# Optimization experiments

Hardware: AMD Instinct MI355X
Metric: run time of the kernel (lower is better)

Reference implementation:

```python
import jax, jax.numpy as jnp
import numpy as np

EPS = 1e-5

def _ln(x, g, b):
    mu = jnp.mean(x, axis=-1, keepdims=True)
    var = jnp.var(x, axis=-1, keepdims=True)
    return (x - mu) * jax.lax.rsqrt(var + EPS) * g + b

def setup_inputs() -> dict:
    key = jax.random.key(0)
    ks = jax.random.split(key, 12)
    T, B, D, H = 64, 2048, 512, 512
    seq = jax.random.normal(ks[0], (T, B, D), dtype=jnp.float32)
    ts = jnp.sort(jax.random.uniform(ks[1], (B, T), dtype=jnp.float32) * 10.0, axis=1)
    def xavier(k, shape):
        fan_in, fan_out = shape[1], shape[0]
        lim = float(np.sqrt(6.0 / (fan_in + fan_out)))
        return jax.random.uniform(k, shape, jnp.float32, -lim, lim)
    Wr = xavier(ks[2], (H, D + H)); br = jnp.ones((H,), jnp.float32)   # reset bias init 1.0
    Wz = xavier(ks[3], (H, D + H)); bz = jnp.ones((H,), jnp.float32)   # update bias init 1.0
    Wc = xavier(ks[4], (H, D + H)); bc = jnp.zeros((H,), jnp.float32)
    Wo = xavier(ks[5], (H, H));     bo = jnp.zeros((H,), jnp.float32)  # output projection
    gx = jnp.ones((D,), jnp.float32); bx = jnp.zeros((D,), jnp.float32)  # layer_norm_x
    gh = jnp.ones((H,), jnp.float32); bh = jnp.zeros((H,), jnp.float32)  # layer_norm_h
    gc = jnp.ones((H,), jnp.float32); bcell = jnp.zeros((H,), jnp.float32)  # layer_norm_out (cell)
    gf = jnp.ones((H,), jnp.float32); bf = jnp.zeros((H,), jnp.float32)  # final layer_norm
    return {"seq": seq, "time_stamps": ts,
            "Wr": Wr, "br": br, "Wz": Wz, "bz": bz, "Wc": Wc, "bc": bc,
            "Wo": Wo, "bo": bo, "gx": gx, "bx": bx, "gh": gh, "bh": bh,
            "gc": gc, "bcell": bcell, "gf": gf, "bf": bf}

def _cell(xn, hn, Wr, br, Wz, bz, Wc, bc, gc, bcell):
    # xn: normalized input [B,D]; hn: (normalized, time-scaled) hidden [B,H]
    xh = jnp.concatenate([xn, hn], axis=-1)
    r = jax.nn.sigmoid(xh @ Wr.T + br)
    z = jax.nn.sigmoid(xh @ Wz.T + bz)
    xrh = jnp.concatenate([xn, r * hn], axis=-1)
    h_tilde = jnp.tanh(xrh @ Wc.T + bc)
    h_new = (1.0 - z) * hn + z * h_tilde
    return _ln(h_new, gc, bcell)  # cell output layer norm (dropout is identity in eval)

def reference(seq, time_stamps, Wr, br, Wz, bz, Wc, bc, Wo, bo, gx, bx, gh, bh, gc, bcell, gf, bf):
    T, B, D = seq.shape
    # first step: h is None -> zeros, no LN on h, no time-decay
    x0 = _ln(seq[0], gx, bx)
    h0 = _cell(x0, jnp.zeros((B, Wr.shape[0]), seq.dtype), Wr, br, Wz, bz, Wc, bc, gc, bcell)
    # remaining steps under scan with LN(h) and exp(-dt) decay
    dts = (time_stamps[:, 1:] - time_stamps[:, :-1]).T  # [T-1, B]
    def step(h, inp):
        x_t, dt = inp
        xn = _ln(x_t, gx, bx)
        hn = _ln(h, gh, bh) * jnp.exp(-jnp.clip(dt, 0.0, 10.0))[:, None]
        h_new = _cell(xn, hn, Wr, br, Wz, bz, Wc, bc, gc, bcell)
        return h_new, h_new
    _, rest = jax.lax.scan(step, h0, (seq[1:], dts))
    states = jnp.concatenate([h0[None], rest], axis=0)  # [T,B,H]
    out = jnp.einsum('tbh,oh->tbo', states, Wo) + bo
    out = out + seq  # residual (input_dim == hidden_dim); dropout identity in eval
    return _ln(out, gf, bf)
```

## Files before the change

### kernel.cpp

```cpp
#include <hip/hip_runtime.h>
#include <math.h>

#define TT 64
#define BB 2048

using f32x4   = __attribute__((ext_vector_type(4))) float;
using short8  = __attribute__((ext_vector_type(8))) short;
using short4v = __attribute__((ext_vector_type(4))) short;

__device__ __forceinline__ unsigned short f2bf(float f) {
    unsigned u = __float_as_uint(f);
    u += 0x7FFF + ((u >> 16) & 1);
    return (unsigned short)(u >> 16);
}
__device__ __forceinline__ float bf2f(unsigned short h) {
    return __uint_as_float(((unsigned)h) << 16);
}
__device__ __forceinline__ float sigmoidf_(float v) { return 1.0f / (1.0f + expf(-v)); }
__device__ __forceinline__ float tanhf_(float v)    { return 1.0f - 2.0f / (expf(2.0f * v) + 1.0f); }

__global__ __launch_bounds__(256)
void cvt_kernel(const float* __restrict__ src, unsigned short* __restrict__ dst, int n) {
    int i = blockIdx.x * 256 + threadIdx.x;
    if (i < n) dst[i] = f2bf(src[i]);
}

__global__ __launch_bounds__(256)
void pack_w2(const float* __restrict__ src, unsigned short* __restrict__ dst,
             int N, int Ksrc, int kbeg, int Kpk) {
    int i = blockIdx.x * 256 + threadIdx.x;
    if (i >= N * Kpk) return;
    int n = i / Kpk, k = i - n * Kpk;
    int dstIdx = ((n >> 4) * (Kpk >> 5) + (k >> 5)) * 512 + (((k >> 3) & 3) * 16 + (n & 15)) * 8 + (k & 7);
    dst[dstIdx] = f2bf(src[(size_t)n * Ksrc + kbeg + k]);
}

__device__ __forceinline__ int pk_idx(int row, int col) {
    int ks = col >> 5, khi = (col >> 3) & 3, j = col & 7;
    return ((ks * 64) + khi * 16 + row) * 8 + j;
}

__device__ __forceinline__ void ln_row_pk(const float* __restrict__ xr,
                                          const float* __restrict__ g,
                                          const float* __restrict__ b,
                                          unsigned short* __restrict__ tile,
                                          int row, int lane) {
    const int c0 = lane * 8;
    float4 v0 = *(const float4*)(xr + c0);
    float4 v1 = *(const float4*)(xr + c0 + 4);
    float s  = v0.x + v0.y + v0.z + v0.w + v1.x + v1.y + v1.z + v1.w;
    float ss = v0.x*v0.x + v0.y*v0.y + v0.z*v0.z + v0.w*v0.w
             + v1.x*v1.x + v1.y*v1.y + v1.z*v1.z + v1.w*v1.w;
#pragma unroll
    for (int m = 32; m > 0; m >>= 1) { s += __shfl_xor(s, m); ss += __shfl_xor(ss, m); }
    const float mean = s * (1.0f / 512.0f);
    const float var  = ss * (1.0f / 512.0f) - mean * mean;
    const float rs   = rsqrtf(var + 1e-5f);
    float4 g0 = *(const float4*)(g + c0);
    float4 g1 = *(const float4*)(g + c0 + 4);
    float4 b0 = *(const float4*)(b + c0);
    float4 b1 = *(const float4*)(b + c0 + 4);
    short8 o;
    o[0] = (short)f2bf((v0.x - mean) * rs * g0.x + b0.x);
    o[1] = (short)f2bf((v0.y - mean) * rs * g0.y + b0.y);
    o[2] = (short)f2bf((v0.z - mean) * rs * g0.z + b0.z);
    o[3] = (short)f2bf((v0.w - mean) * rs * g0.w + b0.w);
    o[4] = (short)f2bf((v1.x - mean) * rs * g1.x + b1.x);
    o[5] = (short)f2bf((v1.y - mean) * rs * g1.y + b1.y);
    o[6] = (short)f2bf((v1.z - mean) * rs * g1.z + b1.z);
    o[7] = (short)f2bf((v1.w - mean) * rs * g1.w + b1.w);
    *(short8*)&tile[(((lane >> 2) * 64) + (lane & 3) * 16 + row) * 8] = o;
}

__global__ __launch_bounds__(512)
void gx_kernel(const float* __restrict__ seq, const float* __restrict__ gxw,
               const float* __restrict__ bxw, const unsigned short* __restrict__ Wx3,
               unsigned short* __restrict__ gx)
{
    __shared__ unsigned short xt[4 * 8192];
    const int tid  = threadIdx.x;
    const int w    = tid >> 6;
    const int lane = tid & 63;
    const size_t m0 = (size_t)blockIdx.x * 64;
    const int t    = (int)(m0 >> 11);
    const int bloc = (int)((m0 & 2047) >> 4);

#pragma unroll
    for (int rr = 0; rr < 8; ++rr) {
        const int r = w * 8 + rr;
        ln_row_pk(seq + (m0 + r) * 512, gxw, bxw, xt + (r >> 4) * 8192, r & 15, lane);
    }
    __syncthreads();

    for (int nt = 0; nt < 3; ++nt) {
        f32x4 acc[4][4] = {};
#pragma unroll 4
        for (int ks = 0; ks < 16; ++ks) {
            short8 a[4], b[4];
#pragma unroll
            for (int mf = 0; mf < 4; ++mf)
                a[mf] = *(const short8*)&xt[mf * 8192 + (ks * 64 + lane) * 8];
#pragma unroll
            for (int nf = 0; nf < 4; ++nf)
                b[nf] = *(const short8*)(Wx3 + (size_t)(nt * 32 + w * 4 + nf) * 8192 + ks * 512 + lane * 8);
#pragma unroll
            for (int mf = 0; mf < 4; ++mf)
#pragma unroll
                for (int nf = 0; nf < 4; ++nf)
                    acc[mf][nf] = __builtin_amdgcn_mfma_f32_16x16x32_bf16(a[mf], b[nf], acc[mf][nf], 0, 0, 0);
        }
#pragma unroll
        for (int mf = 0; mf < 4; ++mf)
#pragma unroll
            for (int nf = 0; nf < 4; ++nf) {
                const size_t base = (((size_t)t * 128 + bloc + mf) * 96 + nt * 32 + w * 4 + nf) * 256 + lane * 4;
                short4v o;
                o[0] = (short)f2bf(acc[mf][nf][0]);
                o[1] = (short)f2bf(acc[mf][nf][1]);
                o[2] = (short)f2bf(acc[mf][nf][2]);
                o[3] = (short)f2bf(acc[mf][nf][3]);
                *(short4v*)&gx[base] = o;
            }
    }
}

template<int SBF, int HOIST>
__global__ __launch_bounds__(512)
void recurrent_kernel(const float* __restrict__ seq, const float* __restrict__ ts,
                      const unsigned short* __restrict__ Wrz, const unsigned short* __restrict__ Wc,
                      const float* __restrict__ br, const float* __restrict__ bz,
                      const float* __restrict__ bc,
                      const float* __restrict__ gxw, const float* __restrict__ bxw,
                      const float* __restrict__ gh, const float* __restrict__ bh,
                      const float* __restrict__ gc, const float* __restrict__ bcl,
                      const unsigned short* __restrict__ gx,
                      float* __restrict__ states_f32, unsigned short* __restrict__ states_bf)
{
    __shared__ unsigned short hn_s[16 * 512];
    __shared__ unsigned short rh_s[16 * 512];
    __shared__ unsigned short xn_s[HOIST ? 64 : 16 * 512];
    __shared__ float red_s[16][8];
    __shared__ float red_q[16][8];

    const int tid  = threadIdx.x;
    const int w    = tid >> 6;
    const int lane = tid & 63;
    const int lhi  = lane >> 4;
    const int llo  = lane & 15;
    const int m0   = blockIdx.x * 16;

    for (int i = tid; i < 1024; i += 512) *(short8*)&hn_s[i * 8] = short8{};
    if (!HOIST) {
#pragma unroll
        for (int rr = 0; rr < 2; ++rr) {
            const int r = w * 2 + rr;
            ln_row_pk(seq + (size_t)(m0 + r) * 512, gxw, bxw, xn_s, r, lane);
        }
    }
    __syncthreads();

    float zreg[4][4];

    for (int t = 0; t < TT; ++t) {
        const unsigned short* gxt = HOIST ? gx + (((size_t)t * 128 + blockIdx.x) * 96) * 256 + lane * 4 : nullptr;

        {
            f32x4 aR[4] = {}, aZ[4] = {};
            if (HOIST) {
#pragma unroll
                for (int f = 0; f < 4; ++f) {
                    short4v g1 = *(const short4v*)(gxt + (size_t)(w * 4 + f) * 256);
                    short4v g2 = *(const short4v*)(gxt + (size_t)(32 + w * 4 + f) * 256);
#pragma unroll
                    for (int i = 0; i < 4; ++i) {
                        aR[f][i] = bf2f((unsigned short)g1[i]);
                        aZ[f][i] = bf2f((unsigned short)g2[i]);
                    }
                }
#pragma unroll 4
                for (int ks = 0; ks < 16; ++ks) {
                    short8 a = *(const short8*)&hn_s[(ks * 64 + lane) * 8];
                    const int off = ks * 512 + lane * 8;
#pragma unroll
                    for (int f = 0; f < 4; ++f) {
                        short8 b1 = *(const short8*)(Wrz + (size_t)(w * 4 + f) * 8192 + off);
                        aR[f] = __builtin_amdgcn_mfma_f32_16x16x32_bf16(a, b1, aR[f], 0, 0, 0);
                        short8 b2 = *(const short8*)(Wrz + (size_t)(32 + w * 4 + f) * 8192 + off);
                        aZ[f] = __builtin_amdgcn_mfma_f32_16x16x32_bf16(a, b2, aZ[f], 0, 0, 0);
                    }
                }
            } else {
                const unsigned short* wrb = Wrz + (size_t)(w * 4) * 16384;
                const unsigned short* wzb = Wrz + (size_t)(32 + w * 4) * 16384;
#pragma unroll 4
                for (int ks = 0; ks < 16; ++ks) {
                    short8 a = *(const short8*)&xn_s[(ks * 64 + lane) * 8];
                    const int off = ks * 512 + lane * 8;
#pragma unroll
                    for (int f = 0; f < 4; ++f) {
                        short8 b1 = *(const short8*)(wrb + (size_t)f * 16384 + off);
                        aR[f] = __builtin_amdgcn_mfma_f32_16x16x32_bf16(a, b1, aR[f], 0, 0, 0);
                        short8 b2 = *(const short8*)(wzb + (size_t)f * 16384 + off);
                        aZ[f] = __builtin_amdgcn_mfma_f32_16x16x32_bf16(a, b2, aZ[f], 0, 0, 0);
                    }
                }
#pragma unroll 4
                for (int ks = 16; ks < 32; ++ks) {
                    short8 a = *(const short8*)&hn_s[((ks - 16) * 64 + lane) * 8];
                    const int off = ks * 512 + lane * 8;
#pragma unroll
                    for (int f = 0; f < 4; ++f) {
                        short8 b1 = *(const short8*)(wrb + (size_t)f * 16384 + off);
                        aR[f] = __builtin_amdgcn_mfma_f32_16x16x32_bf16(a, b1, aR[f], 0, 0, 0);
                        short8 b2 = *(const short8*)(wzb + (size_t)f * 16384 + off);
                        aZ[f] = __builtin_amdgcn_mfma_f32_16x16x32_bf16(a, b2, aZ[f], 0, 0, 0);
                    }
                }
            }
#pragma unroll
            for (int f = 0; f < 4; ++f)
#pragma unroll
                for (int i = 0; i < 4; ++i) {
                    const int row = lhi * 4 + i;
                    const int col = w * 64 + f * 16 + llo;
                    const float rr = sigmoidf_(aR[f][i] + br[col]);
                    const float hv = bf2f(hn_s[pk_idx(row, col)]);
                    rh_s[pk_idx(row, col)] = f2bf(rr * hv);
                    zreg[f][i] = sigmoidf_(aZ[f][i] + bz[col]);
                }
        }
        __syncthreads();

        f32x4 aC[4] = {};
        {
            if (HOIST) {
#pragma unroll
                for (int f = 0; f < 4; ++f) {
                    short4v g3 = *(const short4v*)(gxt + (size_t)(64 + w * 4 + f) * 256);
#pragma unroll
                    for (int i = 0; i < 4; ++i) aC[f][i] = bf2f((unsigned short)g3[i]);
                }
#pragma unroll 4
                for (int ks = 0; ks < 16; ++ks) {
                    short8 a = *(const short8*)&rh_s[(ks * 64 + lane) * 8];
                    const int off = ks * 512 + lane * 8;
#pragma unroll
                    for (int f = 0; f < 4; ++f) {
                        short8 b1 = *(const short8*)(Wc + (size_t)(w * 4 + f) * 8192 + off);
                        aC[f] = __builtin_amdgcn_mfma_f32_16x16x32_bf16(a, b1, aC[f], 0, 0, 0);
                    }
                }
            } else {
                const unsigned short* wcb = Wc + (size_t)(w * 4) * 16384;
#pragma unroll 4
                for (int ks = 0; ks < 16; ++ks) {
                    short8 a = *(const short8*)&xn_s[(ks * 64 + lane) * 8];
                    const int off = ks * 512 + lane * 8;
#pragma unroll
                    for (int f = 0; f < 4; ++f) {
                        short8 b1 = *(const short8*)(wcb + (size_t)f * 16384 + off);
                        aC[f] = __builtin_amdgcn_mfma_f32_16x16x32_bf16(a, b1, aC[f], 0, 0, 0);
                    }
                }
#pragma unroll 4
                for (int ks = 16; ks < 32; ++ks) {
                    short8 a = *(const short8*)&rh_s[((ks - 16) * 64 + lane) * 8];
                    const int off = ks * 512 + lane * 8;
#pragma unroll
                    for (int f = 0; f < 4; ++f) {
                        short8 b1 = *(const short8*)(wcb + (size_t)f * 16384 + off);
                        aC[f] = __builtin_amdgcn_mfma_f32_16x16x32_bf16(a, b1, aC[f], 0, 0, 0);
                    }
                }
            }
        }
        __syncthreads();

        {
            float hnew[4][4];
#pragma unroll
            for (int f = 0; f < 4; ++f)
#pragma unroll
                for (int i = 0; i < 4; ++i) {
                    const int row = lhi * 4 + i;
                    const int col = w * 64 + f * 16 + llo;
                    const float htil = tanhf_(aC[f][i] + bc[col]);
                    const float hv = bf2f(hn_s[pk_idx(row, col)]);
                    const float z = zreg[f][i];
                    hnew[f][i] = (1.0f - z) * hv + z * htil;
                }
#pragma unroll
            for (int i = 0; i < 4; ++i) {
                float s = hnew[0][i] + hnew[1][i] + hnew[2][i] + hnew[3][i];
                float q = hnew[0][i]*hnew[0][i] + hnew[1][i]*hnew[1][i]
                        + hnew[2][i]*hnew[2][i] + hnew[3][i]*hnew[3][i];
#pragma unroll
                for (int m = 8; m >= 1; m >>= 1) { s += __shfl_xor(s, m); q += __shfl_xor(q, m); }
                if (llo == 0) { red_s[lhi * 4 + i][w] = s; red_q[lhi * 4 + i][w] = q; }
            }
            __syncthreads();
            float mu[4], rsd[4];
#pragma unroll
            for (int i = 0; i < 4; ++i) {
                float s = 0.f, q = 0.f;
#pragma unroll
                for (int w2 = 0; w2 < 8; ++w2) { s += red_s[lhi * 4 + i][w2]; q += red_q[lhi * 4 + i][w2]; }
                const float m_ = s * (1.0f / 512.0f);
                mu[i]  = m_;
                rsd[i] = rsqrtf(q * (1.0f / 512.0f) - m_ * m_ + 1e-5f);
            }
#pragma unroll
            for (int f = 0; f < 4; ++f)
#pragma unroll
                for (int i = 0; i < 4; ++i) {
                    const int row = lhi * 4 + i;
                    const int col = w * 64 + f * 16 + llo;
                    const float h = (hnew[f][i] - mu[i]) * rsd[i] * gc[col] + bcl[col];
                    const size_t off = (size_t)t * BB * 512 + (size_t)(m0 + row) * 512 + col;
                    if (SBF) states_bf[off] = f2bf(h);
                    else     states_f32[off] = h;
                    hnew[f][i] = h;
                }
            if (t + 1 < TT) {
                __syncthreads();
#pragma unroll
                for (int i = 0; i < 4; ++i) {
                    float s = hnew[0][i] + hnew[1][i] + hnew[2][i] + hnew[3][i];
                    float q = hnew[0][i]*hnew[0][i] + hnew[1][i]*hnew[1][i]
                            + hnew[2][i]*hnew[2][i] + hnew[3][i]*hnew[3][i];
#pragma unroll
                    for (int m = 8; m >= 1; m >>= 1) { s += __shfl_xor(s, m); q += __shfl_xor(q, m); }
                    if (llo == 0) { red_s[lhi * 4 + i][w] = s; red_q[lhi * 4 + i][w] = q; }
                }
                __syncthreads();
                float dec_[4];
#pragma unroll
                for (int i = 0; i < 4; ++i) {
                    float s = 0.f, q = 0.f;
#pragma unroll
                    for (int w2 = 0; w2 < 8; ++w2) { s += red_s[lhi * 4 + i][w2]; q += red_q[lhi * 4 + i][w2]; }
                    const float m_ = s * (1.0f / 512.0f);
                    mu[i]  = m_;
                    rsd[i] = rsqrtf(q * (1.0f / 512.0f) - m_ * m_ + 1e-5f);
                    const int row = m0 + lhi * 4 + i;
                    float dtv = ts[(size_t)row * TT + t + 1] - ts[(size_t)row * TT + t];
                    dtv = fminf(fmaxf(dtv, 0.0f), 10.0f);
                    dec_[i] = expf(-dtv);
                }
#pragma unroll
                for (int f = 0; f < 4; ++f)
#pragma unroll
                    for (int i = 0; i < 4; ++i) {
                        const int row = lhi * 4 + i;
                        const int col = w * 64 + f * 16 + llo;
                        const float hv = ((hnew[f][i] - mu[i]) * rsd[i] * gh[col] + bh[col]) * dec_[i];
                        hn_s[pk_idx(row, col)] = f2bf(hv);
                    }
                if (!HOIST) {
#pragma unroll
                    for (int rr = 0; rr < 2; ++rr) {
                        const int r = w * 2 + rr;
                        ln_row_pk(seq + ((size_t)(t + 1) * BB + m0 + r) * 512, gxw, bxw, xn_s, r, lane);
                    }
                }
            }
        }
        __syncthreads();
    }
}

template<int BF>
__global__ __launch_bounds__(512)
void proj_kernel(const float* __restrict__ S, const unsigned short* __restrict__ Sb,
                 const unsigned short* __restrict__ Wo, const float* __restrict__ bo,
                 const float* __restrict__ seq, const float* __restrict__ gf,
                 const float* __restrict__ bff, float* __restrict__ out)
{
    const int tid  = threadIdx.x;
    const int wave = tid >> 6;
    const int lane = tid & 63;
    const int lhi  = lane >> 4;
    const int llo  = lane & 15;
    const long m0  = (long)blockIdx.x * 64;

    f32x4 acc[4][4] = {};
    for (int k0 = 0; k0 < 512; k0 += 32) {
        const int kk = k0 + lhi * 8;
        short8 a[4], b[4];
#pragma unroll
        for (int mf = 0; mf < 4; ++mf) {
            if (BF) {
                a[mf] = *(const short8*)(Sb + (size_t)(m0 + mf * 16 + llo) * 512 + kk);
            } else {
                const float* ap = S + (size_t)(m0 + mf * 16 + llo) * 512 + kk;
                float4 f0 = *(const float4*)ap;
                float4 f1 = *(const float4*)(ap + 4);
                short8 av;
                av[0] = (short)f2bf(f0.x); av[1] = (short)f2bf(f0.y);
                av[2] = (short)f2bf(f0.z); av[3] = (short)f2bf(f0.w);
                av[4] = (short)f2bf(f1.x); av[5] = (short)f2bf(f1.y);
                av[6] = (short)f2bf(f1.z); av[7] = (short)f2bf(f1.w);
                a[mf] = av;
            }
        }
#pragma unroll
        for (int nf = 0; nf < 4; ++nf)
            b[nf] = *(const short8*)(Wo + (size_t)(wave * 64 + nf * 16 + llo) * 512 + kk);
#pragma unroll
        for (int mf = 0; mf < 4; ++mf)
#pragma unroll
            for (int nf = 0; nf < 4; ++nf)
                acc[mf][nf] = __builtin_amdgcn_mfma_f32_16x16x32_bf16(a[mf], b[nf], acc[mf][nf], 0, 0, 0);
    }

    __shared__ float red_s[64][8];
    __shared__ float red_q[64][8];

#pragma unroll
    for (int mf = 0; mf < 4; ++mf)
#pragma unroll
        for (int i = 0; i < 4; ++i) {
            const long row = m0 + mf * 16 + lhi * 4 + i;
#pragma unroll
            for (int nf = 0; nf < 4; ++nf) {
                const int col = wave * 64 + nf * 16 + llo;
                acc[mf][nf][i] += bo[col] + seq[(size_t)row * 512 + col];
            }
        }
    float mu[4][4], rstd[4][4];
#pragma unroll
    for (int mf = 0; mf < 4; ++mf)
#pragma unroll
        for (int i = 0; i < 4; ++i) {
            float s = 0.f, q = 0.f;
#pragma unroll
            for (int nf = 0; nf < 4; ++nf) { const float v = acc[mf][nf][i]; s += v; q += v * v; }
#pragma unroll
            for (int m = 8; m >= 1; m >>= 1) { s += __shfl_xor(s, m); q += __shfl_xor(q, m); }
            if (llo == 0) { red_s[mf * 16 + lhi * 4 + i][wave] = s; red_q[mf * 16 + lhi * 4 + i][wave] = q; }
        }
    __syncthreads();
#pragma unroll
    for (int mf = 0; mf < 4; ++mf)
#pragma unroll
        for (int i = 0; i < 4; ++i) {
            const int rl = mf * 16 + lhi * 4 + i;
            float s = 0.f, q = 0.f;
#pragma unroll
            for (int w2 = 0; w2 < 8; ++w2) { s += red_s[rl][w2]; q += red_q[rl][w2]; }
            const float m_ = s * (1.0f / 512.0f);
            const float var = q * (1.0f / 512.0f) - m_ * m_;
            mu[mf][i] = m_;
            rstd[mf][i] = rsqrtf(var + 1e-5f);
        }
#pragma unroll
    for (int mf = 0; mf < 4; ++mf)
#pragma unroll
        for (int i = 0; i < 4; ++i) {
            const long row = m0 + mf * 16 + lhi * 4 + i;
#pragma unroll
            for (int nf = 0; nf < 4; ++nf) {
                const int col = wave * 64 + nf * 16 + llo;
                out[(size_t)row * 512 + col] = (acc[mf][nf][i] - mu[mf][i]) * rstd[mf][i] * gf[col] + bff[col];
            }
        }
}

extern "C" void kernel_launch(void* const* d_in, const int* in_sizes, int n_in,
                              void* d_out, int out_size, void* d_ws, size_t ws_size,
                              hipStream_t stream) {
    const float* seq = (const float*)d_in[0];
    const float* ts  = (const float*)d_in[1];
    const float* Wr  = (const float*)d_in[2];
    const float* br  = (const float*)d_in[3];
    const float* Wz  = (const float*)d_in[4];
    const float* bz  = (const float*)d_in[5];
    const float* Wc  = (const float*)d_in[6];
    const float* bc  = (const float*)d_in[7];
    const float* Wo  = (const float*)d_in[8];
    const float* bo  = (const float*)d_in[9];
    const float* gx  = (const float*)d_in[10];
    const float* bx  = (const float*)d_in[11];
    const float* gh  = (const float*)d_in[12];
    const float* bh  = (const float*)d_in[13];
    const float* gc  = (const float*)d_in[14];
    const float* bcl = (const float*)d_in[15];
    const float* gf  = (const float*)d_in[16];
    const float* bf  = (const float*)d_in[17];
    float* out = (float*)d_out;

    char* w0 = (char*)d_ws;
    char* w = w0;
    unsigned short* Wrz_full = (unsigned short*)w; w += (size_t)1024 * 1024 * 2;
    unsigned short* Wc_full  = (unsigned short*)w; w += (size_t)512 * 1024 * 2;
    unsigned short* Wrz_h    = (unsigned short*)w; w += (size_t)1024 * 512 * 2;
    unsigned short* Wc_h     = (unsigned short*)w; w += (size_t)512 * 512 * 2;
    unsigned short* Wx3      = (unsigned short*)w; w += (size_t)1536 * 512 * 2;
    unsigned short* Wo_b     = (unsigned short*)w; w += (size_t)512 * 512 * 2;

    const size_t GXB = (size_t)TT * 128 * 96 * 256 * 2;
    const size_t SBB = (size_t)TT * BB * 512 * 2;

    const bool hoist = ws_size >= (size_t)(w - w0) + GXB;
    unsigned short* gxbuf = (unsigned short*)w;
    if (hoist) w += GXB;
    const bool sbf = ws_size >= (size_t)(w - w0) + SBB;
    unsigned short* states_bf = (unsigned short*)w;

    if (hoist) {
        pack_w2<<<1024, 256, 0, stream>>>(Wr, Wrz_h, 512, 1024, 512, 512);
        pack_w2<<<1024, 256, 0, stream>>>(Wz, Wrz_h + (size_t)512 * 512, 512, 1024, 512, 512);
        pack_w2<<<1024, 256, 0, stream>>>(Wc, Wc_h, 512, 1024, 512, 512);
        pack_w2<<<1024, 256, 0, stream>>>(Wr, Wx3, 512, 1024, 0, 512);
        pack_w2<<<1024, 256, 0, stream>>>(Wz, Wx3 + (size_t)512 * 512, 512, 1024, 0, 512);
        pack_w2<<<1024, 256, 0, stream>>>(Wc, Wx3 + (size_t)2 * 512 * 512, 512, 1024, 0, 512);
    } else {
        pack_w2<<<2048, 256, 0, stream>>>(Wr, Wrz_full, 512, 1024, 0, 1024);
        pack_w2<<<2048, 256, 0, stream>>>(Wz, Wrz_full + (size_t)512 * 1024, 512, 1024, 0, 1024);
        pack_w2<<<2048, 256, 0, stream>>>(Wc, Wc_full, 512, 1024, 0, 1024);
    }
    cvt_kernel<<<(512 * 512 + 255) / 256, 256, 0, stream>>>(Wo, Wo_b, 512 * 512);

    if (hoist)
        gx_kernel<<<2048, 512, 0, stream>>>(seq, gx, bx, Wx3, gxbuf);

    const unsigned short* Wa = hoist ? Wrz_h : Wrz_full;
    const unsigned short* Wb = hoist ? Wc_h  : Wc_full;
    if (hoist) {
        if (sbf) recurrent_kernel<1,1><<<128, 512, 0, stream>>>(seq, ts, Wa, Wb, br, bz, bc, gx, bx, gh, bh, gc, bcl, gxbuf, out, states_bf);
        else     recurrent_kernel<0,1><<<128, 512, 0, stream>>>(seq, ts, Wa, Wb, br, bz, bc, gx, bx, gh, bh, gc, bcl, gxbuf, out, states_bf);
    } else {
        if (sbf) recurrent_kernel<1,0><<<128, 512, 0, stream>>>(seq, ts, Wa, Wb, br, bz, bc, gx, bx, gh, bh, gc, bcl, gxbuf, out, states_bf);
        else     recurrent_kernel<0,0><<<128, 512, 0, stream>>>(seq, ts, Wa, Wb, br, bz, bc, gx, bx, gh, bh, gc, bcl, gxbuf, out, states_bf);
    }

    if (sbf)
        proj_kernel<1><<<2048, 512, 0, stream>>>(out, states_bf, Wo_b, bo, seq, gf, bf, out);
    else
        proj_kernel<0><<<2048, 512, 0, stream>>>(out, nullptr, Wo_b, bo, seq, gf, bf, out);
}
```

Baseline: 1.877 ms.

## Restructure recurrent step: overlap Z/C GEMMs, fuse dual layernorm, pack states for MFMA

The hoisted recurrent kernel now computes R first, then runs the Z and C gate GEMMs in one loop after a single barrier. It keeps hn in registers and computes both the cell layernorm and the next-step hidden layernorm from a single fused reduction, using precomputed gamma/beta moment sums, which removes a reduction round and its barriers per timestep. States are written in the MFMA-packed bf16 layout via coalesced LDS copies, and Wo is packed the same way, so the projection kernel loads contiguous fragments. The algebraic second-layernorm statistics can lose precision through catastrophic cancellation, and register pressure rises.

New measurement: 3.147 ms. +67.7%, slower.

```diff
diff --git a/kernel.cpp b/kernel.cpp
--- a/kernel.cpp
+++ b/kernel.cpp
@@ -18,12 +18,6 @@
 }
 __device__ __forceinline__ float sigmoidf_(float v) { return 1.0f / (1.0f + expf(-v)); }
 __device__ __forceinline__ float tanhf_(float v)    { return 1.0f - 2.0f / (expf(2.0f * v) + 1.0f); }
-
-__global__ __launch_bounds__(256)
-void cvt_kernel(const float* __restrict__ src, unsigned short* __restrict__ dst, int n) {
-    int i = blockIdx.x * 256 + threadIdx.x;
-    if (i < n) dst[i] = f2bf(src[i]);
-}
 
 __global__ __launch_bounds__(256)
 void pack_w2(const float* __restrict__ src, unsigned short* __restrict__ dst,
@@ -124,23 +118,20 @@
     }
 }
 
-template<int SBF, int HOIST>
+template<int SBF>
 __global__ __launch_bounds__(512)
-void recurrent_kernel(const float* __restrict__ seq, const float* __restrict__ ts,
-                      const unsigned short* __restrict__ Wrz, const unsigned short* __restrict__ Wc,
-                      const float* __restrict__ br, const float* __restrict__ bz,
-                      const float* __restrict__ bc,
-                      const float* __restrict__ gxw, const float* __restrict__ bxw,
-                      const float* __restrict__ gh, const float* __restrict__ bh,
-                      const float* __restrict__ gc, const float* __restrict__ bcl,
-                      const unsigned short* __restrict__ gx,
-                      float* __restrict__ states_f32, unsigned short* __restrict__ states_bf)
+void recurrent_h(const float* __restrict__ ts,
+                 const unsigned short* __restrict__ Wrz, const unsigned short* __restrict__ Wc,
+                 const float* __restrict__ br_, const float* __restrict__ bz_, const float* __restrict__ bc_,
+                 const float* __restrict__ gh_, const float* __restrict__ bh_,
+                 const float* __restrict__ gc_, const float* __restrict__ bcl_,
+                 const unsigned short* __restrict__ gx,
+                 float* __restrict__ states_f32, unsigned short* __restrict__ states_pk)
 {
     __shared__ unsigned short hn_s[16 * 512];
     __shared__ unsigned short rh_s[16 * 512];
-    __shared__ unsigned short xn_s[HOIST ? 64 : 16 * 512];
-    __shared__ float red_s[16][8];
-    __shared__ float red_q[16][8];
+    __shared__ float red6[6][16][9];
+    __shared__ float cpart[5][8];
 
     const int tid  = threadIdx.x;
     const int w    = tid >> 6;
@@ -148,75 +139,242 @@
     const int lhi  = lane >> 4;
     const int llo  = lane & 15;
     const int m0   = blockIdx.x * 16;
+    const int blk  = blockIdx.x;
+
+    *(short8*)&hn_s[tid * 16] = short8{};
+    *(short8*)&hn_s[tid * 16 + 8] = short8{};
+
+    {
+        float g = gc_[tid], b = bcl_[tid];
+        float p[5] = { g, b, g * g, g * b, b * b };
+#pragma unroll
+        for (int m = 32; m > 0; m >>= 1)
+#pragma unroll
+            for (int k = 0; k < 5; ++k) p[k] += __shfl_xor(p[k], m);
+        if (lane == 0)
+#pragma unroll
+            for (int k = 0; k < 5; ++k) cpart[k][w] = p[k];
+    }
+    __syncthreads();
+    float C_gc = 0.f, C_bcl = 0.f, C_g2 = 0.f, C_gb = 0.f, C_b2 = 0.f;
+#pragma unroll
+    for (int w2 = 0; w2 < 8; ++w2) {
+        C_gc += cpart[0][w2]; C_bcl += cpart[1][w2]; C_g2 += cpart[2][w2];
+        C_gb += cpart[3][w2]; C_b2 += cpart[4][w2];
+    }
+
+    float brr[4], bzr[4], bcr[4], gcr[4], bclr[4], ghr[4], bhr[4], g2r[4], gbr[4];
+#pragma unroll
+    for (int f = 0; f < 4; ++f) {
+        const int col = w * 64 + f * 16 + llo;
+        brr[f] = br_[col]; bzr[f] = bz_[col]; bcr[f] = bc_[col];
+        gcr[f] = gc_[col]; bclr[f] = bcl_[col];
+        ghr[f] = gh_[col]; bhr[f] = bh_[col];
+        g2r[f] = gcr[f] * gcr[f]; gbr[f] = gcr[f] * bclr[f];
+    }
+
+    float hnreg[4][4] = {};
+
+    for (int t = 0; t < TT; ++t) {
+        if (SBF && t > 0) {
+            unsigned short* dst = states_pk + ((size_t)(t - 1) * 128 + blk) * 8192 + (size_t)(w * 128 + lane * 2) * 8;
+            const unsigned short* srcl = &rh_s[(w * 128 + lane * 2) * 8];
+            short8 s0 = *(const short8*)srcl;
+            short8 s1 = *(const short8*)(srcl + 8);
+            *(short8*)dst = s0;
+            *(short8*)(dst + 8) = s1;
+        }
+
+        const unsigned short* gxt = gx + ((size_t)t * 128 + blk) * 96 * 256 + lane * 4;
+        short4v gR[4], gZ[4], gC[4];
+#pragma unroll
+        for (int f = 0; f < 4; ++f) {
+            gR[f] = *(const short4v*)(gxt + (size_t)(w * 4 + f) * 256);
+            gZ[f] = *(const short4v*)(gxt + (size_t)(32 + w * 4 + f) * 256);
+            gC[f] = *(const short4v*)(gxt + (size_t)(64 + w * 4 + f) * 256);
+        }
+
+        f32x4 aR[4];
+#pragma unroll
+        for (int f = 0; f < 4; ++f)
+#pragma unroll
+            for (int i = 0; i < 4; ++i) aR[f][i] = bf2f((unsigned short)gR[f][i]);
+#pragma unroll 4
+        for (int ks = 0; ks < 16; ++ks) {
+            short8 a = *(const short8*)&hn_s[(ks * 64 + lane) * 8];
+            const int off = ks * 512 + lane * 8;
+#pragma unroll
+            for (int f = 0; f < 4; ++f) {
+                short8 b1 = *(const short8*)(Wrz + (size_t)(w * 4 + f) * 8192 + off);
+                aR[f] = __builtin_amdgcn_mfma_f32_16x16x32_bf16(a, b1, aR[f], 0, 0, 0);
+            }
+        }
+#pragma unroll
+        for (int f = 0; f < 4; ++f)
+#pragma unroll
+            for (int i = 0; i < 4; ++i) {
+                const int row = lhi * 4 + i;
+                const int col = w * 64 + f * 16 + llo;
+                const float rr = sigmoidf_(aR[f][i] + brr[f]);
+                rh_s[pk_idx(row, col)] = f2bf(rr * hnreg[f][i]);
+            }
+        __syncthreads();
+
+        f32x4 aZ[4], aC[4];
+#pragma unroll
+        for (int f = 0; f < 4; ++f)
+#pragma unroll
+            for (int i = 0; i < 4; ++i) {
+                aZ[f][i] = bf2f((unsigned short)gZ[f][i]);
+                aC[f][i] = bf2f((unsigned short)gC[f][i]);
+            }
+#pragma unroll 4
+        for (int ks = 0; ks < 16; ++ks) {
+            short8 ah = *(const short8*)&hn_s[(ks * 64 + lane) * 8];
+            short8 ar = *(const short8*)&rh_s[(ks * 64 + lane) * 8];
+            const int off = ks * 512 + lane * 8;
+#pragma unroll
+            for (int f = 0; f < 4; ++f) {
+                short8 b1 = *(const short8*)(Wrz + (size_t)(32 + w * 4 + f) * 8192 + off);
+                aZ[f] = __builtin_amdgcn_mfma_f32_16x16x32_bf16(ah, b1, aZ[f], 0, 0, 0);
+                short8 b2 = *(const short8*)(Wc + (size_t)(w * 4 + f) * 8192 + off);
+                aC[f] = __builtin_amdgcn_mfma_f32_16x16x32_bf16(ar, b2, aC[f], 0, 0, 0);
+            }
+        }
+
+        float hnew[4][4];
+#pragma unroll
+        for (int f = 0; f < 4; ++f)
+#pragma unroll
+            for (int i = 0; i < 4; ++i) {
+                const float z    = sigmoidf_(aZ[f][i] + bzr[f]);
+                const float htil = tanhf_(aC[f][i] + bcr[f]);
+                hnew[f][i] = (1.0f - z) * hnreg[f][i] + z * htil;
+            }
+#pragma unroll
+        for (int i = 0; i < 4; ++i) {
+            float P[6] = {};
+#pragma unroll
+            for (int f = 0; f < 4; ++f) {
+                const float h = hnew[f][i];
+                P[0] += h;            P[1] += h * h;
+                P[2] += gcr[f] * h;   P[3] += g2r[f] * h;
+                P[4] += g2r[f] * h * h;
+                P[5] += gbr[f] * h;
+            }
+#pragma unroll
+            for (int m = 8; m >= 1; m >>= 1)
+#pragma unroll
+                for (int k = 0; k < 6; ++k) P[k] += __shfl_xor(P[k], m);
+            if (llo == 0)
+#pragma unroll
+                for (int k = 0; k < 6; ++k) red6[k][lhi * 4 + i][w] = P[k];
+        }
+        __syncthreads();
+
+        float mu1[4], rs1[4], mu2[4], rs2[4], dec_[4];
+#pragma unroll
+        for (int i = 0; i < 4; ++i) {
+            const int row = lhi * 4 + i;
+            float S[6] = {};
+#pragma unroll
+            for (int w2 = 0; w2 < 8; ++w2)
+#pragma unroll
+                for (int k = 0; k < 6; ++k) S[k] += red6[k][row][w2];
+            const float m1 = S[0] * (1.0f / 512.0f);
+            const float v1 = S[1] * (1.0f / 512.0f) - m1 * m1;
+            const float r1 = rsqrtf(v1 + 1e-5f);
+            mu1[i] = m1; rs1[i] = r1;
+            const float m2 = (r1 * (S[2] - m1 * C_gc) + C_bcl) * (1.0f / 512.0f);
+            const float eh2 = (r1 * r1 * (S[4] - 2.0f * m1 * S[3] + m1 * m1 * C_g2)
+                               + 2.0f * r1 * (S[5] - m1 * C_gb) + C_b2) * (1.0f / 512.0f);
+            mu2[i] = m2;
+            rs2[i] = rsqrtf(eh2 - m2 * m2 + 1e-5f);
+            if (t + 1 < TT) {
+                const int grow = m0 + row;
+                float dtv = ts[(size_t)grow * TT + t + 1] - ts[(size_t)grow * TT + t];
+                dtv = fminf(fmaxf(dtv, 0.0f), 10.0f);
+                dec_[i] = expf(-dtv);
+            }
+        }
+#pragma unroll
+        for (int f = 0; f < 4; ++f)
+#pragma unroll
+            for (int i = 0; i < 4; ++i) {
+                const int row = lhi * 4 + i;
+                const int col = w * 64 + f * 16 + llo;
+                const float n = (hnew[f][i] - mu1[i]) * rs1[i];
+                const float h = n * gcr[f] + bclr[f];
+                if (SBF) rh_s[pk_idx(row, col)] = f2bf(h);
+                else     states_f32[(size_t)t * BB * 512 + (size_t)(m0 + row) * 512 + col] = h;
+                if (t + 1 < TT) {
+                    const float hv = ((h - mu2[i]) * rs2[i] * ghr[f] + bhr[f]) * dec_[i];
+                    hnreg[f][i] = hv;
+                    hn_s[pk_idx(row, col)] = f2bf(hv);
+                }
+            }
+        __syncthreads();
+    }
+
+    if (SBF) {
+        unsigned short* dst = states_pk + ((size_t)(TT - 1) * 128 + blk) * 8192 + (size_t)(w * 128 + lane * 2) * 8;
+        const unsigned short* srcl = &rh_s[(w * 128 + lane * 2) * 8];
+        short8 s0 = *(const short8*)srcl;
+        short8 s1 = *(const short8*)(srcl + 8);
+        *(short8*)dst = s0;
+        *(short8*)(dst + 8) = s1;
+    }
+}
+
+template<int SBF>
+__global__ __launch_bounds__(512)
+void recurrent_fb(const float* __restrict__ seq, const float* __restrict__ ts,
+                  const unsigned short* __restrict__ Wrz, const unsigned short* __restrict__ Wc,
+                  const float* __restrict__ br, const float* __restrict__ bz,
+                  const float* __restrict__ bc,
+                  const float* __restrict__ gxw, const float* __restrict__ bxw,
+                  const float* __restrict__ gh, const float* __restrict__ bh,
+                  const float* __restrict__ gc, const float* __restrict__ bcl,
+                  float* __restrict__ states_f32, unsigned short* __restrict__ states_pk)
+{
+    __shared__ unsigned short hn_s[16 * 512];
+    __shared__ unsigned short rh_s[16 * 512];
+    __shared__ unsigned short xn_s[16 * 512];
+    __shared__ float red_s[16][9];
+    __shared__ float red_q[16][9];
+
+    const int tid  = threadIdx.x;
+    const int w    = tid >> 6;
+    const int lane = tid & 63;
+    const int lhi  = lane >> 4;
+    const int llo  = lane & 15;
+    const int m0   = blockIdx.x * 16;
 
     for (int i = tid; i < 1024; i += 512) *(short8*)&hn_s[i * 8] = short8{};
-    if (!HOIST) {
-#pragma unroll
-        for (int rr = 0; rr < 2; ++rr) {
-            const int r = w * 2 + rr;
-            ln_row_pk(seq + (size_t)(m0 + r) * 512, gxw, bxw, xn_s, r, lane);
-        }
+#pragma unroll
+    for (int rr = 0; rr < 2; ++rr) {
+        const int r = w * 2 + rr;
+        ln_row_pk(seq + (size_t)(m0 + r) * 512, gxw, bxw, xn_s, r, lane);
     }
     __syncthreads();
 
-    float zreg[4][4];
-
     for (int t = 0; t < TT; ++t) {
-        const unsigned short* gxt = HOIST ? gx + (((size_t)t * 128 + blockIdx.x) * 96) * 256 + lane * 4 : nullptr;
-
         {
             f32x4 aR[4] = {}, aZ[4] = {};
-            if (HOIST) {
+#pragma unroll 2
+            for (int ks = 0; ks < 32; ++ks) {
+                short8 a = (ks < 16) ? *(const short8*)&xn_s[(ks * 64 + lane) * 8]
+                                     : *(const short8*)&hn_s[((ks - 16) * 64 + lane) * 8];
+                const int off = ks * 512 + lane * 8;
 #pragma unroll
                 for (int f = 0; f < 4; ++f) {
-                    short4v g1 = *(const short4v*)(gxt + (size_t)(w * 4 + f) * 256);
-                    short4v g2 = *(const short4v*)(gxt + (size_t)(32 + w * 4 + f) * 256);
-#pragma unroll
-                    for (int i = 0; i < 4; ++i) {
-                        aR[f][i] = bf2f((unsigned short)g1[i]);
-                        aZ[f][i] = bf2f((unsigned short)g2[i]);
-                    }
-                }
-#pragma unroll 4
-                for (int ks = 0; ks < 16; ++ks) {
-                    short8 a = *(const short8*)&hn_s[(ks * 64 + lane) * 8];
-                    const int off = ks * 512 + lane * 8;
-#pragma unroll
-                    for (int f = 0; f < 4; ++f) {
-                        short8 b1 = *(const short8*)(Wrz + (size_t)(w * 4 + f) * 8192 + off);
-                        aR[f] = __builtin_amdgcn_mfma_f32_16x16x32_bf16(a, b1, aR[f], 0, 0, 0);
-                        short8 b2 = *(const short8*)(Wrz + (size_t)(32 + w * 4 + f) * 8192 + off);
-                        aZ[f] = __builtin_amdgcn_mfma_f32_16x16x32_bf16(a, b2, aZ[f], 0, 0, 0);
-                    }
-                }
-            } else {
-                const unsigned short* wrb = Wrz + (size_t)(w * 4) * 16384;
-                const unsigned short* wzb = Wrz + (size_t)(32 + w * 4) * 16384;
-#pragma unroll 4
-                for (int ks = 0; ks < 16; ++ks) {
-                    short8 a = *(const short8*)&xn_s[(ks * 64 + lane) * 8];
-                    const int off = ks * 512 + lane * 8;
-#pragma unroll
-                    for (int f = 0; f < 4; ++f) {
-                        short8 b1 = *(const short8*)(wrb + (size_t)f * 16384 + off);
-                        aR[f] = __builtin_amdgcn_mfma_f32_16x16x32_bf16(a, b1, aR[f], 0, 0, 0);
-                        short8 b2 = *(const short8*)(wzb + (size_t)f * 16384 + off);
-                        aZ[f] = __builtin_amdgcn_mfma_f32_16x16x32_bf16(a, b2, aZ[f], 0, 0, 0);
-                    }
-                }
-#pragma unroll 4
-                for (int ks = 16; ks < 32; ++ks) {
-                    short8 a = *(const short8*)&hn_s[((ks - 16) * 64 + lane) * 8];
-                    const int off = ks * 512 + lane * 8;
-#pragma unroll
-                    for (int f = 0; f < 4; ++f) {
-                        short8 b1 = *(const short8*)(wrb + (size_t)f * 16384 + off);
-                        aR[f] = __builtin_amdgcn_mfma_f32_16x16x32_bf16(a, b1, aR[f], 0, 0, 0);
-                        short8 b2 = *(const short8*)(wzb + (size_t)f * 16384 + off);
-                        aZ[f] = __builtin_amdgcn_mfma_f32_16x16x32_bf16(a, b2, aZ[f], 0, 0, 0);
-                    }
-                }
-            }
+                    short8 b1 = *(const short8*)(Wrz + (size_t)(w * 4 + f) * 16384 + off);
+                    aR[f] = __builtin_amdgcn_mfma_f32_16x16x32_bf16(a, b1, aR[f], 0, 0, 0);
+                    short8 b2 = *(const short8*)(Wrz + (size_t)(32 + w * 4 + f) * 16384 + off);
+                    aZ[f] = __builtin_amdgcn_mfma_f32_16x16x32_bf16(a, b2, aZ[f], 0, 0, 0);
+                }
+            }
+            float zreg[4][4];
 #pragma unroll
             for (int f = 0; f < 4; ++f)
 #pragma unroll
@@ -228,55 +386,22 @@
                     rh_s[pk_idx(row, col)] = f2bf(rr * hv);
                     zreg[f][i] = sigmoidf_(aZ[f][i] + bz[col]);
                 }
-        }
-        __syncthreads();
-
-        f32x4 aC[4] = {};
-        {
-            if (HOIST) {
+            __syncthreads();
+
+            f32x4 aC[4] = {};
+#pragma unroll 2
+            for (int ks = 0; ks < 32; ++ks) {
+                short8 a = (ks < 16) ? *(const short8*)&xn_s[(ks * 64 + lane) * 8]
+                                     : *(const short8*)&rh_s[((ks - 16) * 64 + lane) * 8];
+                const int off = ks * 512 + lane * 8;
 #pragma unroll
                 for (int f = 0; f < 4; ++f) {
-                    short4v g3 = *(const short4v*)(gxt + (size_t)(64 + w * 4 + f) * 256);
-#pragma unroll
-                    for (int i = 0; i < 4; ++i) aC[f][i] = bf2f((unsigned short)g3[i]);
-                }
-#pragma unroll 4
-                for (int ks = 0; ks < 16; ++ks) {
-                    short8 a = *(const short8*)&rh_s[(ks * 64 + lane) * 8];
-                    const int off = ks * 512 + lane * 8;
-#pragma unroll
-                    for (int f = 0; f < 4; ++f) {
-                        short8 b1 = *(const short8*)(Wc + (size_t)(w * 4 + f) * 8192 + off);
-                        aC[f] = __builtin_amdgcn_mfma_f32_16x16x32_bf16(a, b1, aC[f], 0, 0, 0);
-                    }
-                }
-            } else {
-                const unsigned short* wcb = Wc + (size_t)(w * 4) * 16384;
-#pragma unroll 4
-                for (int ks = 0; ks < 16; ++ks) {
-                    short8 a = *(const short8*)&xn_s[(ks * 64 + lane) * 8];
-                    const int off = ks * 512 + lane * 8;
-#pragma unroll
-                    for (int f = 0; f < 4; ++f) {
-                        short8 b1 = *(const short8*)(wcb + (size_t)f * 16384 + off);
-                        aC[f] = __builtin_amdgcn_mfma_f32_16x16x32_bf16(a, b1, aC[f], 0, 0, 0);
-                    }
-                }
-#pragma unroll 4
-                for (int ks = 16; ks < 32; ++ks) {
-                    short8 a = *(const short8*)&rh_s[((ks - 16) * 64 + lane) * 8];
-                    const int off = ks * 512 + lane * 8;
-#pragma unroll
-                    for (int f = 0; f < 4; ++f) {
-                        short8 b1 = *(const short8*)(wcb + (size_t)f * 16384 + off);
-                        aC[f] = __builtin_amdgcn_mfma_f32_16x16x32_bf16(a, b1, aC[f], 0, 0, 0);
-                    }
-                }
-            }
-        }
-        __syncthreads();
-
-        {
+                    short8 b1 = *(const short8*)(Wc + (size_t)(w * 4 + f) * 16384 + off);
+                    aC[f] = __builtin_amdgcn_mfma_f32_16x16x32_bf16(a, b1, aC[f], 0, 0, 0);
+                }
+            }
+            __syncthreads();
+
             float hnew[4][4];
 #pragma unroll
             for (int f = 0; f < 4; ++f)
@@ -286,8 +411,7 @@
                     const int col = w * 64 + f * 16 + llo;
                     const float htil = tanhf_(aC[f][i] + bc[col]);
                     const float hv = bf2f(hn_s[pk_idx(row, col)]);
-                    const float z = zreg[f][i];
-                    hnew[f][i] = (1.0f - z) * hv + z * htil;
+                    hnew[f][i] = (1.0f - zreg[f][i]) * hv + zreg[f][i] * htil;
                 }
 #pragma unroll
             for (int i = 0; i < 4; ++i) {
@@ -316,9 +440,8 @@
                     const int row = lhi * 4 + i;
                     const int col = w * 64 + f * 16 + llo;
                     const float h = (hnew[f][i] - mu[i]) * rsd[i] * gc[col] + bcl[col];
-                    const size_t off = (size_t)t * BB * 512 + (size_t)(m0 + row) * 512 + col;
-                    if (SBF) states_bf[off] = f2bf(h);
-                    else     states_f32[off] = h;
+                    if (SBF) states_pk[((size_t)t * 128 + blockIdx.x) * 8192 + pk_idx(row, col)] = f2bf(h);
+                    else     states_f32[(size_t)t * BB * 512 + (size_t)(m0 + row) * 512 + col] = h;
                     hnew[f][i] = h;
                 }
             if (t + 1 < TT) {
@@ -342,8 +465,8 @@
                     const float m_ = s * (1.0f / 512.0f);
                     mu[i]  = m_;
                     rsd[i] = rsqrtf(q * (1.0f / 512.0f) - m_ * m_ + 1e-5f);
-                    const int row = m0 + lhi * 4 + i;
-                    float dtv = ts[(size_t)row * TT + t + 1] - ts[(size_t)row * TT + t];
+                    const int grow = m0 + lhi * 4 + i;
+                    float dtv = ts[(size_t)grow * TT + t + 1] - ts[(size_t)grow * TT + t];
                     dtv = fminf(fmaxf(dtv, 0.0f), 10.0f);
                     dec_[i] = expf(-dtv);
                 }
@@ -356,22 +479,20 @@
                         const float hv = ((hnew[f][i] - mu[i]) * rsd[i] * gh[col] + bh[col]) * dec_[i];
                         hn_s[pk_idx(row, col)] = f2bf(hv);
                     }
-                if (!HOIST) {
-#pragma unroll
-                    for (int rr = 0; rr < 2; ++rr) {
-                        const int r = w * 2 + rr;
-                        ln_row_pk(seq + ((size_t)(t + 1) * BB + m0 + r) * 512, gxw, bxw, xn_s, r, lane);
-                    }
-                }
-            }
-        }
-        __syncthreads();
+#pragma unroll
+                for (int rr = 0; rr < 2; ++rr) {
+                    const int r = w * 2 + rr;
+                    ln_row_pk(seq + ((size_t)(t + 1) * BB + m0 + r) * 512, gxw, bxw, xn_s, r, lane);
+                }
+            }
+            __syncthreads();
+        }
     }
 }
 
 template<int BF>
 __global__ __launch_bounds__(512)
-void proj_kernel(const float* __restrict__ S, const unsigned short* __restrict__ Sb,
+void proj_kernel(const float* __restrict__ S, const unsigned short* __restrict__ Spk,
                  const unsigned short* __restrict__ Wo, const float* __restrict__ bo,
                  const float* __restrict__ seq, const float* __restrict__ gf,
                  const float* __restrict__ bff, float* __restrict__ out)
@@ -382,17 +503,19 @@
     const int lhi  = lane >> 4;
     const int llo  = lane & 15;
     const long m0  = (long)blockIdx.x * 64;
+    const int t    = (int)(m0 >> 11);
+    const int blk  = (int)((m0 & 2047) >> 4);
 
     f32x4 acc[4][4] = {};
-    for (int k0 = 0; k0 < 512; k0 += 32) {
-        const int kk = k0 + lhi * 8;
+#pragma unroll 2
+    for (int ks = 0; ks < 16; ++ks) {
         short8 a[4], b[4];
 #pragma unroll
         for (int mf = 0; mf < 4; ++mf) {
             if (BF) {
-                a[mf] = *(const short8*)(Sb + (size_t)(m0 + mf * 16 + llo) * 512 + kk);
+                a[mf] = *(const short8*)(Spk + ((size_t)t * 128 + blk + mf) * 8192 + (ks * 64 + lane) * 8);
             } else {
-                const float* ap = S + (size_t)(m0 + mf * 16 + llo) * 512 + kk;
+                const float* ap = S + (size_t)(m0 + mf * 16 + llo) * 512 + ks * 32 + lhi * 8;
                 float4 f0 = *(const float4*)ap;
                 float4 f1 = *(const float4*)(ap + 4);
                 short8 av;
@@ -405,7 +528,7 @@
         }
 #pragma unroll
         for (int nf = 0; nf < 4; ++nf)
-            b[nf] = *(const short8*)(Wo + (size_t)(wave * 64 + nf * 16 + llo) * 512 + kk);
+            b[nf] = *(const short8*)(Wo + (size_t)(wave * 4 + nf) * 8192 + ks * 512 + lane * 8);
 #pragma unroll
         for (int mf = 0; mf < 4; ++mf)
 #pragma unroll
@@ -413,8 +536,8 @@
                 acc[mf][nf] = __builtin_amdgcn_mfma_f32_16x16x32_bf16(a[mf], b[nf], acc[mf][nf], 0, 0, 0);
     }
 
-    __shared__ float red_s[64][8];
-    __shared__ float red_q[64][8];
+    __shared__ float red_s[64][9];
+    __shared__ float red_q[64][9];
 
 #pragma unroll
     for (int mf = 0; mf < 4; ++mf)
@@ -449,9 +572,8 @@
 #pragma unroll
             for (int w2 = 0; w2 < 8; ++w2) { s += red_s[rl][w2]; q += red_q[rl][w2]; }
             const float m_ = s * (1.0f / 512.0f);
-            const float var = q * (1.0f / 512.0f) - m_ * m_;
             mu[mf][i] = m_;
-            rstd[mf][i] = rsqrtf(var + 1e-5f);
+            rstd[mf][i] = rsqrtf(q * (1.0f / 512.0f) - m_ * m_ + 1e-5f);
         }
 #pragma unroll
     for (int mf = 0; mf < 4; ++mf)
@@ -496,16 +618,16 @@
     unsigned short* Wrz_h    = (unsigned short*)w; w += (size_t)1024 * 512 * 2;
     unsigned short* Wc_h     = (unsigned short*)w; w += (size_t)512 * 512 * 2;
     unsigned short* Wx3      = (unsigned short*)w; w += (size_t)1536 * 512 * 2;
-    unsigned short* Wo_b     = (unsigned short*)w; w += (size_t)512 * 512 * 2;
+    unsigned short* Wo_pk    = (unsigned short*)w; w += (size_t)512 * 512 * 2;
 
     const size_t GXB = (size_t)TT * 128 * 96 * 256 * 2;
-    const size_t SBB = (size_t)TT * BB * 512 * 2;
+    const size_t SBB = (size_t)TT * 128 * 8192 * 2;
 
     const bool hoist = ws_size >= (size_t)(w - w0) + GXB;
     unsigned short* gxbuf = (unsigned short*)w;
     if (hoist) w += GXB;
     const bool sbf = ws_size >= (size_t)(w - w0) + SBB;
-    unsigned short* states_bf = (unsigned short*)w;
+    unsigned short* states_pk = (unsigned short*)w;
 
     if (hoist) {
         pack_w2<<<1024, 256, 0, stream>>>(Wr, Wrz_h, 512, 1024, 512, 512);
@@ -519,23 +641,21 @@
         pack_w2<<<2048, 256, 0, stream>>>(Wz, Wrz_full + (size_t)512 * 1024, 512, 1024, 0, 1024);
         pack_w2<<<2048, 256, 0, stream>>>(Wc, Wc_full, 512, 1024, 0, 1024);
     }
-    cvt_kernel<<<(512 * 512 + 255) / 256, 256, 0, stream>>>(Wo, Wo_b, 512 * 512);
+    pack_w2<<<1024, 256, 0, stream>>>(Wo, Wo_pk, 512, 512, 0, 512);
 
     if (hoist)
         gx_kernel<<<2048, 512, 0, stream>>>(seq, gx, bx, Wx3, gxbuf);
 
-    const unsigned short* Wa = hoist ? Wrz_h : Wrz_full;
-    const unsigned short* Wb = hoist ? Wc_h  : Wc_full;
     if (hoist) {
-        if (sbf) recurrent_kernel<1,1><<<128, 512, 0, stream>>>(seq, ts, Wa, Wb, br, bz, bc, gx, bx, gh, bh, gc, bcl, gxbuf, out, states_bf);
-        else     recurrent_kernel<0,1><<<128, 512, 0, stream>>>(seq, ts, Wa, Wb, br, bz, bc, gx, bx, gh, bh, gc, bcl, gxbuf, out, states_bf);
+        if (sbf) recurrent_h<1><<<128, 512, 0, stream>>>(ts, Wrz_h, Wc_h, br, bz, bc, gh, bh, gc, bcl, gxbuf, out, states_pk);
+        else     recurrent_h<0><<<128, 512, 0, stream>>>(ts, Wrz_h, Wc_h, br, bz, bc, gh, bh, gc, bcl, gxbuf, out, states_pk);
     } else {
-        if (sbf) recurrent_kernel<1,0><<<128, 512, 0, stream>>>(seq, ts, Wa, Wb, br, bz, bc, gx, bx, gh, bh, gc, bcl, gxbuf, out, states_bf);
-        else     recurrent_kernel<0,0><<<128, 512, 0, stream>>>(seq, ts, Wa, Wb, br, bz, bc, gx, bx, gh, bh, gc, bcl, gxbuf, out, states_bf);
+        if (sbf) recurrent_fb<1><<<128, 512, 0, stream>>>(seq, ts, Wrz_full, Wc_full, br, bz, bc, gx, bx, gh, bh, gc, bcl, out, states_pk);
+        else     recurrent_fb<0><<<128, 512, 0, stream>>>(seq, ts, Wrz_full, Wc_full, br, bz, bc, gx, bx, gh, bh, gc, bcl, out, states_pk);
     }
 
     if (sbf)
-        proj_kernel<1><<<2048, 512, 0, stream>>>(out, states_bf, Wo_b, bo, seq, gf, bf, out);
+        proj_kernel<1><<<2048, 512, 0, stream>>>(nullptr, states_pk, Wo_pk, bo, seq, gf, bf, out);
     else
-        proj_kernel<0><<<2048, 512, 0, stream>>>(out, nullptr, Wo_b, bo, seq, gf, bf, out);
-}
+        proj_kernel<0><<<2048, 512, 0, stream>>>(out, nullptr, Wo_pk, bo, seq, gf, bf, out);
+}
```
